# Optimization experiments

Hardware: AMD Instinct MI355X
Metric: run time of the kernel (lower is better)

Reference implementation:

```python
import jax, jax.numpy as jnp
import numpy as np

B, W, H, V, L = 64, 512, 1024, 32000, 2


def setup_inputs() -> dict:
    key = jax.random.key(0)
    ks = jax.random.split(key, 20)
    s = 0.02  # init scale
    n = lambda k, shp: jax.random.normal(k, shp, jnp.float32)
    return {
        "input": jax.random.randint(ks[0], (B, 1), 0, V),
        "h0": n(ks[1], (L, B, H)),
        "c0": n(ks[2], (L, B, H)),
        "encoder_output": n(ks[3], (B, W, H)),
        "embedding": n(ks[4], (V, H)) * s,
        "W_ih0": n(ks[5], (4 * H, H)) * s,
        "W_hh0": n(ks[6], (4 * H, H)) * s,
        "b_ih0": n(ks[7], (4 * H,)) * s,
        "b_hh0": n(ks[8], (4 * H,)) * s,
        "W_ih1": n(ks[9], (4 * H, H)) * s,
        "W_hh1": n(ks[10], (4 * H, H)) * s,
        "b_ih1": n(ks[11], (4 * H,)) * s,
        "b_hh1": n(ks[12], (4 * H,)) * s,
        "att_w": n(ks[13], (2 * H,)) * s,
        "att_b": n(ks[14], (1,)) * s,
        "input_W": n(ks[15], (H, 2 * H)) * s,
        "input_b": n(ks[16], (H,)) * s,
        "out_W": n(ks[17], (V, H)) * s,
        "out_b": n(ks[18], (V,)) * s,
    }


def _lstm_step(x, h, c, W_ih, W_hh, b_ih, b_hh):
    # PyTorch gate order: i, f, g, o
    g = x @ W_ih.T + h @ W_hh.T + b_ih + b_hh
    i, f, gg, o = jnp.split(g, 4, axis=-1)
    c2 = jax.nn.sigmoid(f) * c + jax.nn.sigmoid(i) * jnp.tanh(gg)
    return jax.nn.sigmoid(o) * jnp.tanh(c2), c2


def reference(input, h0, c0, encoder_output, embedding,
              W_ih0, W_hh0, b_ih0, b_hh0, W_ih1, W_hh1, b_ih1, b_hh1,
              att_w, att_b, input_W, input_b, out_W, out_b):
    Hd = h0.shape[-1]
    emb = embedding[input]                       # (B,1,H)
    att_state = h0[-1] * c0[-1]                  # (B,H)
    # Vectorized replacement of the per-word cat+linear loop:
    # att_line(cat(enc_w, att_state)) = enc_w @ w_enc + att_state @ w_st + b
    w_enc, w_st = att_w[:Hd], att_w[Hd:]
    scores = encoder_output @ w_enc + (att_state @ w_st)[:, None] + att_b[0]  # (B,W)
    # Original quirk: weigth starts with a zeros column, then softmax over
    # weigth[:, 0:-1] -> zero column + scores for words 0..W-2 (last dropped).
    zeros = jnp.zeros((scores.shape[0], 1), scores.dtype)
    full = jnp.concatenate([zeros, scores[:, :-1]], axis=1)  # (B,W)
    wts = jax.nn.softmax(full, axis=1)
    ctx = jnp.einsum('bw,bwh->bh', wts, encoder_output)      # (B,H)
    x = jnp.concatenate([ctx, emb[:, 0, :]], axis=-1)        # (B,2H)
    x = x @ input_W.T + input_b                              # (B,H)
    h1, c1 = _lstm_step(x, h0[0], c0[0], W_ih0, W_hh0, b_ih0, b_hh0)
    h2, c2 = _lstm_step(h1, h0[1], c0[1], W_ih1, W_hh1, b_ih1, b_hh1)
    logits = h2 @ out_W.T + out_b                            # (B,V)
    logp = jax.nn.log_softmax(logits, axis=-1)[:, None, :]   # (B,1,V)
    return logp, jnp.stack([h1, h2]), jnp.stack([c1, c2])
```

## Files before the change

kernel.cpp:

```cpp
#include <hip/hip_runtime.h>
#include <hip/hip_bf16.h>

#define Bsz 64
#define Wln 512
#define Hd  1024
#define Vc  32000

typedef short v8s __attribute__((ext_vector_type(8)));
typedef float f32x4 __attribute__((ext_vector_type(4)));

__device__ inline unsigned short f2b(float f) {
  union { float f; unsigned u; } v; v.f = f;
  return (unsigned short)((v.u + 0x8000u) >> 16);
}
__device__ inline float wave_sum(float v) {
  #pragma unroll
  for (int o = 32; o; o >>= 1) v += __shfl_down(v, o);
  return v;
}
__device__ inline float wave_max(float v) {
  #pragma unroll
  for (int o = 32; o; o >>= 1) v = fmaxf(v, __shfl_down(v, o));
  return v;
}
__device__ inline float wave_sum_all(float v) {
  #pragma unroll
  for (int o = 32; o; o >>= 1) v += __shfl_xor(v, o);
  return v;
}
__device__ inline float wave_max_all(float v) {
  #pragma unroll
  for (int o = 32; o; o >>= 1) v = fmaxf(v, __shfl_xor(v, o));
  return v;
}
__device__ inline float sigm(float x) { return 1.f / (1.f + expf(-x)); }

__device__ inline v8s cvt_frag(float4 x0, float4 x1) {
  v8s r;
  r[0] = (short)f2b(x0.x); r[1] = (short)f2b(x0.y);
  r[2] = (short)f2b(x0.z); r[3] = (short)f2b(x0.w);
  r[4] = (short)f2b(x1.x); r[5] = (short)f2b(x1.y);
  r[6] = (short)f2b(x1.z); r[7] = (short)f2b(x1.w);
  return r;
}

__device__ inline void stage_A(const float* __restrict__ A, const float* __restrict__ Ab,
                               int sA, char* pool, int tid) {
  #pragma unroll
  for (int it = 0; it < 16; ++it) {
    int idx = it * 512 + tid;
    int row = idx >> 7, ch = idx & 127;
    const float* src = A + (size_t)row * sA + ch * 8;
    float4 x0 = *(const float4*)src;
    float4 x1 = *(const float4*)(src + 4);
    if (Ab) {
      const float* s2 = Ab + (size_t)row * sA + ch * 8;
      float4 y0 = *(const float4*)s2;
      float4 y1 = *(const float4*)(s2 + 4);
      x0.x += y0.x; x0.y += y0.y; x0.z += y0.z; x0.w += y0.w;
      x1.x += y1.x; x1.y += y1.y; x1.z += y1.z; x1.w += y1.w;
    }
    *(v8s*)(pool + row * 2048 + ((ch * 16) ^ ((row & 7) << 4))) = cvt_frag(x0, x1);
  }
}

__global__ __launch_bounds__(256) void k_scores_satt(
    const float* __restrict__ enc, const float* __restrict__ att_w,
    const float* __restrict__ h0, const float* __restrict__ c0,
    const float* __restrict__ att_b, const int* __restrict__ input,
    const float* __restrict__ emb,
    float* __restrict__ scores, float* __restrict__ s_att,
    float* __restrict__ cat)
{
  __shared__ float red[4];
  int t = threadIdx.x;
  if (blockIdx.x < 8192) {
    int row = blockIdx.x * 4 + (t >> 6);
    int lane = t & 63;
    const float* p = enc + (size_t)row * Hd + lane * 16;
    const float* w = att_w + lane * 16;
    float s = 0.f;
    #pragma unroll
    for (int c = 0; c < 4; ++c) {
      float4 e = *(const float4*)(p + c * 4);
      float4 ww = *(const float4*)(w + c * 4);
      s += e.x * ww.x + e.y * ww.y + e.z * ww.z + e.w * ww.w;
    }
    s = wave_sum(s);
    if (lane == 0) scores[row] = s;
  } else {
    int b = blockIdx.x - 8192;
    int idx = input[b];
    for (int j = t; j < Hd; j += 256)
      cat[b * 2 * Hd + Hd + j] = emb[(size_t)idx * Hd + j];
    size_t base = (size_t)(Bsz + b) * Hd;
    float s = 0.f;
    for (int j = t; j < Hd; j += 256)
      s += h0[base + j] * c0[base + j] * att_w[Hd + j];
    s = wave_sum(s);
    if ((t & 63) == 0) red[t >> 6] = s;
    __syncthreads();
    if (t == 0) s_att[b] = red[0] + red[1] + red[2] + red[3] + att_b[0];
  }
}

__global__ __launch_bounds__(512) void k_ctx(
    const float* __restrict__ scores, const float* __restrict__ s_att,
    const float* __restrict__ enc, float* __restrict__ cat)
{
  __shared__ float w_sh[Wln];
  __shared__ float part[8][256];
  __shared__ float redA[8], redB[8];
  int b = blockIdx.x >> 2, qtr = blockIdx.x & 3;
  int tid = threadIdx.x, w = tid >> 6, lane = tid & 63;
  float sa = s_att[b];
  const float* sr = scores + b * Wln;
  float v = (tid == 0) ? 0.f : sr[tid - 1] + sa;
  float m = wave_max(v);
  if (lane == 0) redA[w] = m;
  __syncthreads();
  float M = redA[0];
  #pragma unroll
  for (int i = 1; i < 8; ++i) M = fmaxf(M, redA[i]);
  float e = expf(v - M);
  float s = wave_sum(e);
  if (lane == 0) redB[w] = s;
  __syncthreads();
  float S = redB[0];
  #pragma unroll
  for (int i = 1; i < 8; ++i) S += redB[i];
  w_sh[tid] = e / S;
  __syncthreads();

  const float* pb = enc + (size_t)b * Wln * Hd + qtr * 256 + lane * 4;
  float a0 = 0, a1 = 0, a2 = 0, a3 = 0;
  #pragma unroll 4
  for (int i = 0; i < 64; ++i) {
    int row = w * 64 + i;
    float4 ev = *(const float4*)(pb + (size_t)row * Hd);
    float wi = w_sh[row];
    a0 += wi * ev.x; a1 += wi * ev.y; a2 += wi * ev.z; a3 += wi * ev.w;
  }
  part[w][lane * 4 + 0] = a0; part[w][lane * 4 + 1] = a1;
  part[w][lane * 4 + 2] = a2; part[w][lane * 4 + 3] = a3;
  __syncthreads();
  if (tid < 256) {
    float s2 = 0.f;
    #pragma unroll
    for (int ww = 0; ww < 8; ++ww) s2 += part[ww][tid];
    cat[b * 2 * Hd + qtr * 256 + tid] = s2;
  }
}

__global__ __launch_bounds__(512) void k_input_gemm(
    const float* __restrict__ cat, const float* __restrict__ inW,
    const float* __restrict__ inb, float* __restrict__ x1, float* __restrict__ x2)
{
  __shared__ __align__(16) char pool[131072];
  const int tid = threadIdx.x;
  const int w = tid >> 6, lane = tid & 63;
  const int r = lane & 15, q = lane >> 4;
  const int kh = w;
  const int half = (blockIdx.x >= 64);
  const int n0 = (blockIdx.x & 63) * 16;
  const float* A = cat + half * 1024;
  const float* B = inW + half * 1024;
  float* out = half ? x2 : x1;

  const float* bp = B + (size_t)(n0 + r) * 2048 + kh * 128 + q * 8;
  float4 breg[4][2];
  #pragma unroll
  for (int kk = 0; kk < 4; ++kk) {
    breg[kk][0] = *(const float4*)(bp + kk * 32);
    breg[kk][1] = *(const float4*)(bp + kk * 32 + 4);
  }
  stage_A(A, nullptr, 2048, pool, tid);
  __syncthreads();

  f32x4 acc[4] = {{0,0,0,0},{0,0,0,0},{0,0,0,0},{0,0,0,0}};
  const int swz = (r & 7) << 4;
  #pragma unroll
  for (int kk = 0; kk < 4; ++kk) {
    v8s bf = cvt_frag(breg[kk][0], breg[kk][1]);
    int cb = ((kh * 128 + kk * 32 + q * 8) * 2) ^ swz;
    #pragma unroll
    for (int m = 0; m < 4; ++m) {
      v8s af = *(const v8s*)(pool + (m * 16 + r) * 2048 + cb);
      acc[m] = __builtin_amdgcn_mfma_f32_16x16x32_bf16(af, bf, acc[m], 0, 0, 0);
    }
  }
  __syncthreads();

  float (*red)[64][17] = (float(*)[64][17])pool;
  #pragma unroll
  for (int m = 0; m < 4; ++m)
    #pragma unroll
    for (int rr = 0; rr < 4; ++rr)
      red[w][lane][m * 4 + rr] = acc[m][rr];
  __syncthreads();

  #pragma unroll
  for (int it = 0; it < 2; ++it) {
    int e = it * 512 + tid;
    int cc = e & 15, rowi = e >> 4;
    int idx = ((rowi >> 4) << 2) + (rowi & 3);
    int le  = (((rowi >> 2) & 3) << 4) + cc;
    float s = 0.f;
    #pragma unroll
    for (int j = 0; j < 8; ++j) s += red[j][le][idx];
    float bb = half ? 0.f : inb[n0 + cc];
    out[(size_t)rowi * Hd + n0 + cc] = s + bb;
  }
}

__global__ __launch_bounds__(512) void k_gate_lstm(
    const float* __restrict__ xA, const float* __restrict__ xAb,
    const float* __restrict__ hA,
    const float* __restrict__ W_ih, const float* __restrict__ W_hh,
    const float* __restrict__ b_ih, const float* __restrict__ b_hh,
    const float* __restrict__ c0,
    float* __restrict__ out_h, float* __restrict__ out_c)
{
  __shared__ __align__(16) char pool[131072];
  const int tid = threadIdx.x;
  const int w = tid >> 6, lane = tid & 63;
  const int r = lane & 15, q = lane >> 4;
  const int kh = w;
  const int gate = r >> 2, jl = r & 3;
  const size_t Brow = (size_t)gate * Hd + blockIdx.x * 4 + jl;

  f32x4 acc[4] = {{0,0,0,0},{0,0,0,0},{0,0,0,0},{0,0,0,0}};
  const float* Amat[2] = { xA, hA };
  const float* Abm[2]  = { xAb, nullptr };
  const float* Wmat[2] = { W_ih, W_hh };
  #pragma unroll
  for (int p = 0; p < 2; ++p) {
    const float* bp = Wmat[p] + Brow * Hd + kh * 128 + q * 8;
    float4 breg[4][2];
    #pragma unroll
    for (int kk = 0; kk < 4; ++kk) {
      breg[kk][0] = *(const float4*)(bp + kk * 32);
      breg[kk][1] = *(const float4*)(bp + kk * 32 + 4);
    }
    stage_A(Amat[p], Abm[p], Hd, pool, tid);
    __syncthreads();
    const int swz = (r & 7) << 4;
    #pragma unroll
    for (int kk = 0; kk < 4; ++kk) {
      v8s bf = cvt_frag(breg[kk][0], breg[kk][1]);
      int cb = ((kh * 128 + kk * 32 + q * 8) * 2) ^ swz;
      #pragma unroll
      for (int m = 0; m < 4; ++m) {
        v8s af = *(const v8s*)(pool + (m * 16 + r) * 2048 + cb);
        acc[m] = __builtin_amdgcn_mfma_f32_16x16x32_bf16(af, bf, acc[m], 0, 0, 0);
      }
    }
    __syncthreads();
  }

  float (*red)[64][17] = (float(*)[64][17])pool;
  #pragma unroll
  for (int m = 0; m < 4; ++m)
    #pragma unroll
    for (int rr = 0; rr < 4; ++rr)
      red[w][lane][m * 4 + rr] = acc[m][rr];
  __syncthreads();

  if (tid < 256) {
    int b = tid >> 2, jl2 = tid & 3;
    int jg = blockIdx.x * 4 + jl2;
    float gv[4];
    #pragma unroll
    for (int g2 = 0; g2 < 4; ++g2) {
      int cc = g2 * 4 + jl2;
      int idx = ((b >> 4) << 2) + (b & 3);
      int le  = (((b >> 2) & 3) << 4) + cc;
      float s = 0.f;
      #pragma unroll
      for (int j = 0; j < 8; ++j) s += red[j][le][idx];
      gv[g2] = s + b_ih[(size_t)g2 * Hd + jg] + b_hh[(size_t)g2 * Hd + jg];
    }
    float c = sigm(gv[1]) * c0[(size_t)b * Hd + jg] + sigm(gv[0]) * tanhf(gv[2]);
    float h = sigm(gv[3]) * tanhf(c);
    out_h[(size_t)b * Hd + jg] = h;
    out_c[(size_t)b * Hd + jg] = c;
  }
}

__global__ __launch_bounds__(512) void k_logits(
    const float* __restrict__ A, const float* __restrict__ B,
    const float* __restrict__ bias, float* __restrict__ out,
    float* __restrict__ pm, float* __restrict__ ps)
{
  __shared__ __align__(16) char pool[131072];
  const int tid = threadIdx.x;
  const int w = tid >> 6, lane = tid & 63;
  const int r = lane & 15, q = lane >> 4;
  const int nsub = w & 3, kh = w >> 2;
  const int n0 = blockIdx.x * 64;

  const float* bp = B + (size_t)(n0 + nsub * 16 + r) * Hd + kh * 512 + q * 8;
  float4 breg[16][2];
  #pragma unroll
  for (int kk = 0; kk < 16; ++kk) {
    breg[kk][0] = *(const float4*)(bp + kk * 32);
    breg[kk][1] = *(const float4*)(bp + kk * 32 + 4);
  }
  stage_A(A, nullptr, Hd, pool, tid);
  __syncthreads();

  f32x4 acc[4] = {{0,0,0,0},{0,0,0,0},{0,0,0,0},{0,0,0,0}};
  const int swz = (r & 7) << 4;
  #pragma unroll
  for (int kk = 0; kk < 16; ++kk) {
    v8s bf = cvt_frag(breg[kk][0], breg[kk][1]);
    int cb = ((kh * 512 + kk * 32 + q * 8) * 2) ^ swz;
    #pragma unroll
    for (int m = 0; m < 4; ++m) {
      v8s af = *(const v8s*)(pool + (m * 16 + r) * 2048 + cb);
      acc[m] = __builtin_amdgcn_mfma_f32_16x16x32_bf16(af, bf, acc[m], 0, 0, 0);
    }
  }
  __syncthreads();

  float (*red)[64][17] = (float(*)[64][17])pool;
  #pragma unroll
  for (int m = 0; m < 4; ++m)
    #pragma unroll
    for (int rr = 0; rr < 4; ++rr)
      red[w][lane][m * 4 + rr] = acc[m][rr];
  __syncthreads();

  #pragma unroll
  for (int it = 0; it < 8; ++it) {
    int e = it * 512 + tid;
    int cc = e & 63, rowi = e >> 6;
    int ns2 = cc >> 4, lo = cc & 15;
    int idx = ((rowi >> 4) << 2) + (rowi & 3);
    int le  = (((rowi >> 2) & 3) << 4) + lo;
    float val = red[ns2][le][idx] + red[ns2 + 4][le][idx] + bias[n0 + cc];
    out[(size_t)rowi * Vc + n0 + cc] = val;
    float wm = wave_max_all(val);
    float we = wave_sum_all(expf(val - wm));
    if (cc == 0) { pm[blockIdx.x * 64 + rowi] = wm; ps[blockIdx.x * 64 + rowi] = we; }
  }
}

__global__ __launch_bounds__(512) void k_lsm_sub(
    float* __restrict__ lg, const float* __restrict__ pm, const float* __restrict__ ps)
{
  __shared__ float redA[8], redB[8];
  int b = blockIdx.x >> 2, qc = blockIdx.x & 3;
  int tid = threadIdx.x, w = tid >> 6, lane = tid & 63;
  float m = -1e30f;
  for (int j = tid; j < 500; j += 512) m = fmaxf(m, pm[j * 64 + b]);
  m = wave_max(m);
  if (lane == 0) redA[w] = m;
  __syncthreads();
  float M = redA[0];
  #pragma unroll
  for (int i = 1; i < 8; ++i) M = fmaxf(M, redA[i]);
  float s = 0.f;
  for (int j = tid; j < 500; j += 512) s += ps[j * 64 + b] * expf(pm[j * 64 + b] - M);
  s = wave_sum(s);
  if (lane == 0) redB[w] = s;
  __syncthreads();
  float S = redB[0];
  #pragma unroll
  for (int i = 1; i < 8; ++i) S += redB[i];
  float lse = M + logf(S);
  float* row = lg + (size_t)b * Vc + qc * 8000;
  for (int j = tid * 4; j < 8000; j += 2048) {
    float4 v = *(const float4*)(row + j);
    v.x -= lse; v.y -= lse; v.z -= lse; v.w -= lse;
    *(float4*)(row + j) = v;
  }
}

extern "C" void kernel_launch(void* const* d_in, const int* in_sizes, int n_in,
                              void* d_out, int out_size, void* d_ws, size_t ws_size,
                              hipStream_t stream)
{
  const int*   input = (const int*)d_in[0];
  const float* h0    = (const float*)d_in[1];
  const float* c0    = (const float*)d_in[2];
  const float* enc   = (const float*)d_in[3];
  const float* emb   = (const float*)d_in[4];
  const float* W_ih0 = (const float*)d_in[5];
  const float* W_hh0 = (const float*)d_in[6];
  const float* b_ih0 = (const float*)d_in[7];
  const float* b_hh0 = (const float*)d_in[8];
  const float* W_ih1 = (const float*)d_in[9];
  const float* W_hh1 = (const float*)d_in[10];
  const float* b_ih1 = (const float*)d_in[11];
  const float* b_hh1 = (const float*)d_in[12];
  const float* att_w = (const float*)d_in[13];
  const float* att_b = (const float*)d_in[14];
  const float* inW   = (const float*)d_in[15];
  const float* inb   = (const float*)d_in[16];
  const float* outW  = (const float*)d_in[17];
  const float* outb  = (const float*)d_in[18];
  float* out = (float*)d_out;

  char* ws = (char*)d_ws;
  float* cat    = (float*)(ws + 0);
  float* x1     = (float*)(ws + 524288);
  float* x2     = (float*)(ws + 786432);
  float* scores = (float*)(ws + 1048576);
  float* s_att  = (float*)(ws + 1179648);
  float* pm     = (float*)(ws + 1180672);
  float* ps     = (float*)(ws + 1310720);

  float* out_h = out + (size_t)Bsz * Vc;
  float* out_c = out_h + 2 * Bsz * Hd;
  float* h1 = out_h;
  float* h2 = out_h + Bsz * Hd;

  k_scores_satt<<<8256, 256, 0, stream>>>(enc, att_w, h0, c0, att_b, input, emb,
                                          scores, s_att, cat);
  k_ctx<<<Bsz * 4, 512, 0, stream>>>(scores, s_att, enc, cat);
  k_input_gemm<<<128, 512, 0, stream>>>(cat, inW, inb, x1, x2);
  k_gate_lstm<<<256, 512, 0, stream>>>(x1, x2, h0, W_ih0, W_hh0, b_ih0, b_hh0,
                                       c0, h1, out_c);
  k_gate_lstm<<<256, 512, 0, stream>>>(h1, nullptr, h0 + (size_t)Bsz * Hd,
                                       W_ih1, W_hh1, b_ih1, b_hh1,
                                       c0 + (size_t)Bsz * Hd, h2, out_c + Bsz * Hd);
  k_logits<<<500, 512, 0, stream>>>(h2, outW, outb, out, pm, ps);
  k_lsm_sub<<<256, 512, 0, stream>>>(out, pm, ps);
}
```

Measured before the change: 143.7 us.

## Fuse attention scores, softmax and context into one split-softmax kernel

Replaces the separate scores and context kernels with a single kernel per (batch, 64-row chunk). Each chunk computes its scores, a local max and exp-sum, and a partial context from the same encoder rows, so the encoder is read once while it is likely still in cache instead of twice. A small finalize kernel rescales the eight chunk partials with the global max and sum, and also copies the embedding row. The cost is an extra partial-context buffer in the workspace, an extra tiny launch, and a large shared-memory reduction array that may limit occupancy.

```diff
diff --git a/kernel.cpp b/kernel.cpp
--- a/kernel.cpp
+++ b/kernel.cpp
@@ -64,92 +64,113 @@
   }
 }
 
-__global__ __launch_bounds__(256) void k_scores_satt(
+__global__ __launch_bounds__(512) void k_attn(
     const float* __restrict__ enc, const float* __restrict__ att_w,
     const float* __restrict__ h0, const float* __restrict__ c0,
-    const float* __restrict__ att_b, const int* __restrict__ input,
-    const float* __restrict__ emb,
-    float* __restrict__ scores, float* __restrict__ s_att,
-    float* __restrict__ cat)
-{
-  __shared__ float red[4];
-  int t = threadIdx.x;
-  if (blockIdx.x < 8192) {
-    int row = blockIdx.x * 4 + (t >> 6);
-    int lane = t & 63;
-    const float* p = enc + (size_t)row * Hd + lane * 16;
-    const float* w = att_w + lane * 16;
+    const float* __restrict__ att_b,
+    float* __restrict__ ctxp, float* __restrict__ pm_a, float* __restrict__ ps_a)
+{
+  __shared__ float fullv[64];
+  __shared__ float redA[8];
+  __shared__ float red[8][64][17];
+  const int b = blockIdx.x >> 3, ch = blockIdx.x & 7;
+  const int tid = threadIdx.x, w = tid >> 6, lane = tid & 63;
+
+  {
+    size_t base = (size_t)(Bsz + b) * Hd;
+    int j = tid * 2;
+    float s = h0[base + j] * c0[base + j] * att_w[Hd + j]
+            + h0[base + j + 1] * c0[base + j + 1] * att_w[Hd + j + 1];
+    s = wave_sum(s);
+    if (lane == 0) redA[w] = s;
+  }
+  __syncthreads();
+  float sa = att_b[0];
+  #pragma unroll
+  for (int i = 0; i < 8; ++i) sa += redA[i];
+
+  const float* aw = att_w + lane * 16;
+  float4 w0 = *(const float4*)aw,       w1 = *(const float4*)(aw + 4);
+  float4 w2 = *(const float4*)(aw + 8), w3 = *(const float4*)(aw + 12);
+  const float* encb = enc + (size_t)b * Wln * Hd;
+  const int r = ch * 64 + w * 8;
+
+  #pragma unroll
+  for (int k = 0; k < 8; ++k) {
+    int i = r + k;
+    float v = 0.f;
+    if (i > 0) {
+      const float* p = encb + (size_t)(i - 1) * Hd + lane * 16;
+      float4 e0 = *(const float4*)p,       e1 = *(const float4*)(p + 4);
+      float4 e2 = *(const float4*)(p + 8), e3 = *(const float4*)(p + 12);
+      float s = e0.x*w0.x + e0.y*w0.y + e0.z*w0.z + e0.w*w0.w
+              + e1.x*w1.x + e1.y*w1.y + e1.z*w1.z + e1.w*w1.w
+              + e2.x*w2.x + e2.y*w2.y + e2.z*w2.z + e2.w*w2.w
+              + e3.x*w3.x + e3.y*w3.y + e3.z*w3.z + e3.w*w3.w;
+      s = wave_sum(s);
+      v = s + sa;
+    }
+    if (lane == 0) fullv[w * 8 + k] = v;
+  }
+  __syncthreads();
+
+  float mv = fullv[lane];
+  float M = wave_max_all(mv);
+  float S = wave_sum_all(expf(mv - M));
+
+  float a[16];
+  #pragma unroll
+  for (int ii = 0; ii < 16; ++ii) a[ii] = 0.f;
+  #pragma unroll
+  for (int k = 0; k < 8; ++k) {
+    float wt = expf(fullv[w * 8 + k] - M);
+    const float* p = encb + (size_t)(r + k) * Hd + lane * 16;
+    float4 e0 = *(const float4*)p,       e1 = *(const float4*)(p + 4);
+    float4 e2 = *(const float4*)(p + 8), e3 = *(const float4*)(p + 12);
+    a[0] += wt * e0.x; a[1] += wt * e0.y; a[2]  += wt * e0.z; a[3]  += wt * e0.w;
+    a[4] += wt * e1.x; a[5] += wt * e1.y; a[6]  += wt * e1.z; a[7]  += wt * e1.w;
+    a[8] += wt * e2.x; a[9] += wt * e2.y; a[10] += wt * e2.z; a[11] += wt * e2.w;
+    a[12]+= wt * e3.x; a[13]+= wt * e3.y; a[14] += wt * e3.z; a[15] += wt * e3.w;
+  }
+  #pragma unroll
+  for (int ii = 0; ii < 16; ++ii) red[w][lane][ii] = a[ii];
+  __syncthreads();
+
+  for (int c = tid; c < Hd; c += 512) {
     float s = 0.f;
     #pragma unroll
-    for (int c = 0; c < 4; ++c) {
-      float4 e = *(const float4*)(p + c * 4);
-      float4 ww = *(const float4*)(w + c * 4);
-      s += e.x * ww.x + e.y * ww.y + e.z * ww.z + e.w * ww.w;
-    }
-    s = wave_sum(s);
-    if (lane == 0) scores[row] = s;
-  } else {
-    int b = blockIdx.x - 8192;
-    int idx = input[b];
-    for (int j = t; j < Hd; j += 256)
-      cat[b * 2 * Hd + Hd + j] = emb[(size_t)idx * Hd + j];
-    size_t base = (size_t)(Bsz + b) * Hd;
+    for (int ww = 0; ww < 8; ++ww) s += red[ww][c >> 4][c & 15];
+    ctxp[((size_t)b * 8 + ch) * Hd + c] = s;
+  }
+  if (tid == 0) { pm_a[b * 8 + ch] = M; ps_a[b * 8 + ch] = S; }
+}
+
+__global__ __launch_bounds__(512) void k_ctx_fin(
+    const float* __restrict__ ctxp, const float* __restrict__ pm_a,
+    const float* __restrict__ ps_a, const int* __restrict__ input,
+    const float* __restrict__ emb, float* __restrict__ cat)
+{
+  int b = blockIdx.x, tid = threadIdx.x;
+  float Mg = pm_a[b * 8];
+  #pragma unroll
+  for (int c = 1; c < 8; ++c) Mg = fmaxf(Mg, pm_a[b * 8 + c]);
+  float Sg = 0.f;
+  float sc[8];
+  #pragma unroll
+  for (int c = 0; c < 8; ++c) {
+    sc[c] = expf(pm_a[b * 8 + c] - Mg);
+    Sg += ps_a[b * 8 + c] * sc[c];
+  }
+  float inv = 1.f / Sg;
+  for (int h = tid; h < Hd; h += 512) {
     float s = 0.f;
-    for (int j = t; j < Hd; j += 256)
-      s += h0[base + j] * c0[base + j] * att_w[Hd + j];
-    s = wave_sum(s);
-    if ((t & 63) == 0) red[t >> 6] = s;
-    __syncthreads();
-    if (t == 0) s_att[b] = red[0] + red[1] + red[2] + red[3] + att_b[0];
-  }
-}
-
-__global__ __launch_bounds__(512) void k_ctx(
-    const float* __restrict__ scores, const float* __restrict__ s_att,
-    const float* __restrict__ enc, float* __restrict__ cat)
-{
-  __shared__ float w_sh[Wln];
-  __shared__ float part[8][256];
-  __shared__ float redA[8], redB[8];
-  int b = blockIdx.x >> 2, qtr = blockIdx.x & 3;
-  int tid = threadIdx.x, w = tid >> 6, lane = tid & 63;
-  float sa = s_att[b];
-  const float* sr = scores + b * Wln;
-  float v = (tid == 0) ? 0.f : sr[tid - 1] + sa;
-  float m = wave_max(v);
-  if (lane == 0) redA[w] = m;
-  __syncthreads();
-  float M = redA[0];
-  #pragma unroll
-  for (int i = 1; i < 8; ++i) M = fmaxf(M, redA[i]);
-  float e = expf(v - M);
-  float s = wave_sum(e);
-  if (lane == 0) redB[w] = s;
-  __syncthreads();
-  float S = redB[0];
-  #pragma unroll
-  for (int i = 1; i < 8; ++i) S += redB[i];
-  w_sh[tid] = e / S;
-  __syncthreads();
-
-  const float* pb = enc + (size_t)b * Wln * Hd + qtr * 256 + lane * 4;
-  float a0 = 0, a1 = 0, a2 = 0, a3 = 0;
-  #pragma unroll 4
-  for (int i = 0; i < 64; ++i) {
-    int row = w * 64 + i;
-    float4 ev = *(const float4*)(pb + (size_t)row * Hd);
-    float wi = w_sh[row];
-    a0 += wi * ev.x; a1 += wi * ev.y; a2 += wi * ev.z; a3 += wi * ev.w;
-  }
-  part[w][lane * 4 + 0] = a0; part[w][lane * 4 + 1] = a1;
-  part[w][lane * 4 + 2] = a2; part[w][lane * 4 + 3] = a3;
-  __syncthreads();
-  if (tid < 256) {
-    float s2 = 0.f;
-    #pragma unroll
-    for (int ww = 0; ww < 8; ++ww) s2 += part[ww][tid];
-    cat[b * 2 * Hd + qtr * 256 + tid] = s2;
-  }
+    #pragma unroll
+    for (int c = 0; c < 8; ++c) s += ctxp[((size_t)b * 8 + c) * Hd + h] * sc[c];
+    cat[b * 2 * Hd + h] = s * inv;
+  }
+  int idx = input[b];
+  for (int j = tid; j < Hd; j += 512)
+    cat[b * 2 * Hd + Hd + j] = emb[(size_t)idx * Hd + j];
 }
 
 __global__ __launch_bounds__(512) void k_input_gemm(
@@ -406,19 +427,19 @@
   float* cat    = (float*)(ws + 0);
   float* x1     = (float*)(ws + 524288);
   float* x2     = (float*)(ws + 786432);
-  float* scores = (float*)(ws + 1048576);
-  float* s_att  = (float*)(ws + 1179648);
-  float* pm     = (float*)(ws + 1180672);
-  float* ps     = (float*)(ws + 1310720);
+  float* ctxp   = (float*)(ws + 1048576);
+  float* pm_a   = (float*)(ws + 3145728);
+  float* ps_a   = (float*)(ws + 3147776);
+  float* pm     = (float*)(ws + 3149824);
+  float* ps     = (float*)(ws + 3280896);
 
   float* out_h = out + (size_t)Bsz * Vc;
   float* out_c = out_h + 2 * Bsz * Hd;
   float* h1 = out_h;
   float* h2 = out_h + Bsz * Hd;
 
-  k_scores_satt<<<8256, 256, 0, stream>>>(enc, att_w, h0, c0, att_b, input, emb,
-                                          scores, s_att, cat);
-  k_ctx<<<Bsz * 4, 512, 0, stream>>>(scores, s_att, enc, cat);
+  k_attn<<<Bsz * 8, 512, 0, stream>>>(enc, att_w, h0, c0, att_b, ctxp, pm_a, ps_a);
+  k_ctx_fin<<<Bsz, 512, 0, stream>>>(ctxp, pm_a, ps_a, input, emb, cat);
   k_input_gemm<<<128, 512, 0, stream>>>(cat, inW, inb, x1, x2);
   k_gate_lstm<<<256, 512, 0, stream>>>(x1, x2, h0, W_ih0, W_hh0, b_ih0, b_hh0,
                                        c0, h1, out_c);
```

After: 204.7 us. 42.4% more time.
